# Kernel optimization log

Hardware: AMD Instinct MI355X
Metric: run time of the kernel (lower is better)

The kernel has to match this reference:

```python
import jax, jax.numpy as jnp
import numpy as np

N = 100000   # nodes
E = 3200000  # edges
HIGH, LOW, EMB, HID, OUT = 384, 64, 128, 128, 2

def setup_inputs() -> dict:
    key = jax.random.key(0)
    ks = jax.random.split(key, 12)
    def lin(k, fan_in, fan_out):
        bound = 1.0 / np.sqrt(fan_in)
        kw, kb = jax.random.split(k)
        W = jax.random.uniform(kw, (fan_in, fan_out), jnp.float32, -bound, bound)
        b = jax.random.uniform(kb, (fan_out,), jnp.float32, -bound, bound)
        return W, b
    W_emb, b_emb = lin(ks[0], LOW, EMB)
    W1, b1 = lin(ks[1], HIGH + EMB, HID)
    W2, b2 = lin(ks[2], HID, HID)
    W_lin, b_lin = lin(ks[3], HID, OUT)
    return {
        "high_dim_features": jax.random.normal(ks[4], (N, HIGH), jnp.float32),
        "low_dim_features": jax.random.normal(ks[5], (N, LOW), jnp.float32),
        "edge_index": jax.random.randint(ks[6], (2, E), 0, N, jnp.int32),
        "W_emb": W_emb, "b_emb": b_emb,
        "W1": W1, "b1": b1,
        "W2": W2, "b2": b2,
        "W_lin": W_lin, "b_lin": b_lin,
    }

def _gcn_conv(x, W, b, src, dst, dis):
    # GCNConv: add self-loops, symmetric normalization D^-1/2 (A+I) D^-1/2
    xl = x @ W                                   # [N, out]
    norm = dis[src] * dis[dst]                   # [E]
    agg = jax.ops.segment_sum(xl[src] * norm[:, None], dst, num_segments=N)
    agg = agg + xl * (dis * dis)[:, None]        # self-loop term
    return agg + b

def reference(high_dim_features, low_dim_features, edge_index,
              W_emb, b_emb, W1, b1, W2, b2, W_lin, b_lin):
    src, dst = edge_index[0], edge_index[1]
    # degree with self-loops, computed on destination nodes (PyG default)
    deg = jax.ops.segment_sum(jnp.ones((E,), jnp.float32), dst, num_segments=N) + 1.0
    dis = jax.lax.rsqrt(deg)                     # deg >= 1 always

    low_emb = jax.nn.relu(low_dim_features @ W_emb + b_emb)
    x = jnp.concatenate([high_dim_features, low_emb], axis=1)  # [N, HIGH+EMB]
    x = jax.nn.relu(_gcn_conv(x, W1, b1, src, dst, dis))
    # dropout is identity in eval mode
    x = jax.nn.relu(_gcn_conv(x, W2, b2, src, dst, dis))
    x = x @ W_lin + b_lin
    return jax.nn.log_softmax(x, axis=1)
```

## Files before the change

### kernel.cpp

```cpp
#include <hip/hip_runtime.h>

#define HIGH 384
#define LOWD 64
#define EMB  128
#define HID  128

#define BINSHIFT 8
#define SRCBITS  17
#define SRCMASK  0x1FFFF
#define NBLK     256

typedef unsigned int u32;
typedef unsigned short u16;
typedef unsigned char u8;
typedef __attribute__((ext_vector_type(8))) short bf16x8;
typedef __attribute__((ext_vector_type(4))) float f32x4;
typedef __attribute__((ext_vector_type(2))) float f32x2;

__device__ __forceinline__ u32 pack_bf16(float a, float b) {
    u32 ua = __builtin_bit_cast(u32, a);
    u32 ub = __builtin_bit_cast(u32, b);
    ua += 0x7fffu + ((ua >> 16) & 1u);
    ub += 0x7fffu + ((ub >> 16) & 1u);
    return (ua >> 16) | (ub & 0xffff0000u);
}
__device__ __forceinline__ u16 pack1_bf16(float a) {
    u32 ua = __builtin_bit_cast(u32, a);
    ua += 0x7fffu + ((ua >> 16) & 1u);
    return (u16)(ua >> 16);
}
__device__ __forceinline__ u8 pack1_fp8(float a) {
    int r = __builtin_amdgcn_cvt_pk_fp8_f32(a, a, 0, false);
    return (u8)(r & 0xff);
}


__global__ void k_dis(const int* __restrict__ cnt, float* __restrict__ dis, int N) {
    int i = blockIdx.x * 256 + threadIdx.x;
    if (i < N) dis[i] = rsqrtf((float)cnt[i] + 1.0f);
}

__global__ void k_castw_all(const float* __restrict__ W1, u16* __restrict__ Wt1,
                            const float* __restrict__ W2, u16* __restrict__ Wt2,
                            const float* __restrict__ WE, u16* __restrict__ WtE) {
    int i = blockIdx.x * 256 + threadIdx.x;
    if (i < 65536) {
        int k = i >> 7, c = i & 127;
        Wt1[c * 512 + k] = pack1_bf16(W1[i]);
    } else if (i < 81920) {
        int j = i - 65536;
        int k = j >> 7, c = j & 127;
        Wt2[c * 128 + k] = pack1_bf16(W2[j]);
    } else if (i < 90112) {
        int j = i - 81920;
        int k = j >> 7, c = j & 127;
        WtE[c * 64 + k] = pack1_bf16(WE[j]);
    }
}


__global__ __launch_bounds__(256) void k_binhist(const int* __restrict__ dst, int E,
                                                 int* __restrict__ cnts, int NB) {
    __shared__ int hist[512];
    for (int b = threadIdx.x; b < NB; b += 256) hist[b] = 0;
    __syncthreads();
    int CH = (E + gridDim.x - 1) / gridDim.x;
    int e0 = blockIdx.x * CH;
    int e1 = min(E, e0 + CH);
    for (int e = e0 + threadIdx.x; e < e1; e += 256)
        atomicAdd(&hist[dst[e] >> BINSHIFT], 1);
    __syncthreads();
    for (int b = threadIdx.x; b < NB; b += 256)
        cnts[b * NBLK + blockIdx.x] = hist[b];
}

__global__ __launch_bounds__(256) void k_binscatter(const int* __restrict__ src,
                                                    const int* __restrict__ dst, int E,
                                                    const int* __restrict__ cnts,
                                                    u32* __restrict__ packed, int NB) {
    __shared__ int cur[512];
    for (int b = threadIdx.x; b < NB; b += 256) cur[b] = cnts[b * NBLK + blockIdx.x];
    __syncthreads();
    int CH = (E + gridDim.x - 1) / gridDim.x;
    int e0 = blockIdx.x * CH;
    int e1 = min(E, e0 + CH);
    for (int e = e0 + threadIdx.x; e < e1; e += 256) {
        int d = dst[e];
        int s = src[e];
        int bin = d >> BINSHIFT;
        int pos = atomicAdd(&cur[bin], 1);
        packed[pos] = (u32)s | ((u32)(d & 255) << SRCBITS);
    }
}

__global__ __launch_bounds__(256) void k_hist2(const u32* __restrict__ packed,
                                               const int* __restrict__ cnts, int E,
                                               int* __restrict__ cnt, int NB, int N) {
    __shared__ int hist[256];
    int t = threadIdx.x;
    hist[t] = 0;
    __syncthreads();
    int b = blockIdx.x;
    int begin = cnts[b * NBLK];
    int end = (b + 1 < NB) ? cnts[(b + 1) * NBLK] : E;
    for (int e = begin + t; e < end; e += 256)
        atomicAdd(&hist[packed[e] >> SRCBITS], 1);
    __syncthreads();
    int idx = (b << BINSHIFT) + t;
    if (idx < N) cnt[idx] = hist[t];
}

__global__ __launch_bounds__(256) void k_fill2(const u32* __restrict__ packed,
                                               const int* __restrict__ cnts, int E,
                                               const int* __restrict__ row_start,
                                               int* __restrict__ csr, int NB, int N) {
    __shared__ int cur[256];
    int t = threadIdx.x;
    int b = blockIdx.x;
    int base = b << BINSHIFT;
    cur[t] = row_start[min(base + t, N)];
    __syncthreads();
    int begin = cnts[b * NBLK];
    int end = (b + 1 < NB) ? cnts[(b + 1) * NBLK] : E;
    for (int e = begin + t; e < end; e += 256) {
        u32 p = packed[e];
        int pos = atomicAdd(&cur[p >> SRCBITS], 1);
        csr[pos] = (int)((p & SRCMASK) << 5);
    }
}


__global__ void k_scan1(const int* __restrict__ in, int n, int* __restrict__ bsums) {
    __shared__ int sh[256];
    int t = threadIdx.x;
    int base = blockIdx.x * 1024 + t * 4;
    int s = 0;
#pragma unroll
    for (int j = 0; j < 4; j++) { int idx = base + j; s += (idx < n) ? in[idx] : 0; }
    sh[t] = s; __syncthreads();
    for (int off = 128; off > 0; off >>= 1) {
        if (t < off) sh[t] += sh[t + off];
        __syncthreads();
    }
    if (t == 0) bsums[blockIdx.x] = sh[0];
}

__global__ void k_scan2(int* bsums, int nb) {
    if (threadIdx.x == 0 && blockIdx.x == 0) {
        int run = 0;
        for (int i = 0; i < nb; i++) { int v = bsums[i]; bsums[i] = run; run += v; }
    }
}

__global__ void k_scan3_flat(int* __restrict__ data, int n, const int* __restrict__ bsums) {
    __shared__ int sh[256];
    int t = threadIdx.x;
    int base = blockIdx.x * 1024 + t * 4;
    int v[4]; int s = 0;
#pragma unroll
    for (int j = 0; j < 4; j++) { int idx = base + j; v[j] = (idx < n) ? data[idx] : 0; s += v[j]; }
    sh[t] = s; __syncthreads();
    int x = s;
    for (int off = 1; off < 256; off <<= 1) {
        int y = (t >= off) ? sh[t - off] : 0;
        __syncthreads();
        x += y; sh[t] = x;
        __syncthreads();
    }
    int run = bsums[blockIdx.x] + (x - s);
#pragma unroll
    for (int j = 0; j < 4; j++) {
        int idx = base + j;
        if (idx < n) data[idx] = run;
        run += v[j];
    }
}

__global__ void k_scan3_rows(const int* __restrict__ cnt, int N, const int* __restrict__ bsums,
                             int* __restrict__ row_start, int E) {
    __shared__ int sh[256];
    int t = threadIdx.x;
    int base = blockIdx.x * 1024 + t * 4;
    int v[4]; int s = 0;
#pragma unroll
    for (int j = 0; j < 4; j++) { int idx = base + j; v[j] = (idx < N) ? cnt[idx] : 0; s += v[j]; }
    sh[t] = s; __syncthreads();
    int x = s;
    for (int off = 1; off < 256; off <<= 1) {
        int y = (t >= off) ? sh[t - off] : 0;
        __syncthreads();
        x += y; sh[t] = x;
        __syncthreads();
    }
    int run = bsums[blockIdx.x] + (x - s);
#pragma unroll
    for (int j = 0; j < 4; j++) {
        int idx = base + j;
        if (idx < N) row_start[idx] = run;
        run += v[j];
    }
    if (blockIdx.x == 0 && t == 0) row_start[N] = E;
}


template<bool A1BF, bool BIAS, bool RELU, bool SCALE, int OUT>
__global__ __launch_bounds__(256) void k_mgemm(
    const void* __restrict__ A1v, int K1,
    const u32* __restrict__ A2, int K2,
    const u16* __restrict__ Wt,
    const float* __restrict__ bias,
    const float* __restrict__ dis,
    void* __restrict__ Cv, int M)
{
    __shared__ u32 Als[2][128][16];
    __shared__ u32 Bls[2][128][16];

    const int tid = threadIdx.x;
    const int l = tid & 63;
    const int w = tid >> 6;
    const int g = l >> 4;
    const int lr = l & 15;
    const int blockRow = blockIdx.x * 128;
    const int K = K1 + K2;
    const int T = K >> 5;

    const int sr = tid >> 1;
    const int sh_ = tid & 1;
    int arow = blockRow + sr; if (arow >= M) arow = M - 1;
    const int ssw = (sr >> 1) & 3;
    const int sb0 = (sh_ * 2 + ssw) & 3;
    const int sb1 = (sh_ * 2 + 1 + ssw) & 3;

    const float* a1f = (const float*)A1v + (size_t)arow * K1;
    const u32*   a1b = (const u32*)A1v + (size_t)arow * (K1 >> 1);
    const u32*   a2b = A2 + (size_t)arow * (K2 >> 1);
    const u32*   wtb = (const u32*)Wt + (size_t)sr * (K >> 1);

    f32x4 acc[2][8];
#pragma unroll
    for (int i = 0; i < 2; i++)
#pragma unroll
        for (int j = 0; j < 8; j++) acc[i][j] = (f32x4)0.f;

    u32 pk[8], wk[8];

    auto load_tile = [&](int k0) {
        if (k0 < K1) {
            if (A1BF) {
                const u32* src = a1b + ((k0 + sh_ * 16) >> 1);
                uint4 a = *(const uint4*)src;
                uint4 b = *(const uint4*)(src + 4);
                pk[0] = a.x; pk[1] = a.y; pk[2] = a.z; pk[3] = a.w;
                pk[4] = b.x; pk[5] = b.y; pk[6] = b.z; pk[7] = b.w;
            } else {
                const float* src = a1f + k0 + sh_ * 16;
                float4 f0 = *(const float4*)(src + 0);
                float4 f1 = *(const float4*)(src + 4);
                float4 f2 = *(const float4*)(src + 8);
                float4 f3 = *(const float4*)(src + 12);
                pk[0] = pack_bf16(f0.x, f0.y); pk[1] = pack_bf16(f0.z, f0.w);
                pk[2] = pack_bf16(f1.x, f1.y); pk[3] = pack_bf16(f1.z, f1.w);
                pk[4] = pack_bf16(f2.x, f2.y); pk[5] = pack_bf16(f2.z, f2.w);
                pk[6] = pack_bf16(f3.x, f3.y); pk[7] = pack_bf16(f3.z, f3.w);
            }
        } else {
            const u32* src = a2b + ((k0 - K1 + sh_ * 16) >> 1);
            uint4 a = *(const uint4*)src;
            uint4 b = *(const uint4*)(src + 4);
            pk[0] = a.x; pk[1] = a.y; pk[2] = a.z; pk[3] = a.w;
            pk[4] = b.x; pk[5] = b.y; pk[6] = b.z; pk[7] = b.w;
        }
        const u32* srcw = wtb + ((k0 + sh_ * 16) >> 1);
        uint4 a = *(const uint4*)srcw;
        uint4 b = *(const uint4*)(srcw + 4);
        wk[0] = a.x; wk[1] = a.y; wk[2] = a.z; wk[3] = a.w;
        wk[4] = b.x; wk[5] = b.y; wk[6] = b.z; wk[7] = b.w;
    };
    auto store_tile = [&](int buf) {
        *(uint4*)&Als[buf][sr][sb0 * 4] = make_uint4(pk[0], pk[1], pk[2], pk[3]);
        *(uint4*)&Als[buf][sr][sb1 * 4] = make_uint4(pk[4], pk[5], pk[6], pk[7]);
        *(uint4*)&Bls[buf][sr][sb0 * 4] = make_uint4(wk[0], wk[1], wk[2], wk[3]);
        *(uint4*)&Bls[buf][sr][sb1 * 4] = make_uint4(wk[4], wk[5], wk[6], wk[7]);
    };

    load_tile(0);
    store_tile(0);
    __syncthreads();

    for (int t = 0; t < T; t++) {
        const int cur = t & 1;
        const bool more = (t + 1 < T);
        if (more) load_tile((t + 1) << 5);

        bf16x8 af[2];
#pragma unroll
        for (int rf = 0; rf < 2; rf++) {
            int r = w * 32 + rf * 16 + lr;
            int blk = (g + ((r >> 1) & 3)) & 3;
            af[rf] = *(const bf16x8*)&Als[cur][r][blk * 4];
        }
#pragma unroll
        for (int cb = 0; cb < 8; cb++) {
            int c = cb * 16 + lr;
            int blk = (g + ((c >> 1) & 3)) & 3;
            bf16x8 bf = *(const bf16x8*)&Bls[cur][c][blk * 4];
            acc[0][cb] = __builtin_amdgcn_mfma_f32_16x16x32_bf16(af[0], bf, acc[0][cb], 0, 0, 0);
            acc[1][cb] = __builtin_amdgcn_mfma_f32_16x16x32_bf16(af[1], bf, acc[1][cb], 0, 0, 0);
        }
        if (more) store_tile(cur ^ 1);
        __syncthreads();
    }

    float disv[2][4];
    if (SCALE) {
#pragma unroll
        for (int rf = 0; rf < 2; rf++)
#pragma unroll
            for (int j = 0; j < 4; j++) {
                int row = blockRow + w * 32 + rf * 16 + g * 4 + j;
                disv[rf][j] = (row < M) ? dis[row] : 0.f;
            }
    }
#pragma unroll
    for (int rf = 0; rf < 2; rf++) {
#pragma unroll
        for (int cb = 0; cb < 8; cb++) {
            int col = cb * 16 + lr;
            float bv = BIAS ? bias[col] : 0.f;
#pragma unroll
            for (int j = 0; j < 4; j++) {
                int row = blockRow + w * 32 + rf * 16 + g * 4 + j;
                if (row < M) {
                    float v = acc[rf][cb][j];
                    if (BIAS) v += bv;
                    if (SCALE) v *= disv[rf][j];
                    if (RELU) v = fmaxf(v, 0.f);
                    if (OUT == 0) {
                        ((u16*)Cv)[(size_t)row * 128 + col] = pack1_bf16(v);
                    } else {
                        ((u8*)Cv)[(size_t)row * 128 + col] = pack1_fp8(v);
                    }
                }
            }
        }
    }
}


template<int MODE>
__global__ __launch_bounds__(256) void k_gatherw(
    const u32* __restrict__ xls32, const int* __restrict__ row_start,
    const int* __restrict__ csr, const float* __restrict__ dis,
    const float* __restrict__ bias, const float* __restrict__ Wl,
    const float* __restrict__ bl, void* __restrict__ outv, int N)
{
    int wave = threadIdx.x >> 6;
    int lane = threadIdx.x & 63;
    int half = lane >> 5;
    int w32 = lane & 31;
    int n = blockIdx.x * 4 + wave;
    if (n >= N) return;
    int jb = row_start[n], je = row_start[n + 1];

    float a0 = 0.f, a1 = 0.f, a2 = 0.f, a3 = 0.f;
    {
        u32 v = xls32[(u32)n * 32 + w32];
        if (half == 0) {
            f32x2 lo = __builtin_amdgcn_cvt_pk_f32_fp8((int)v, false);
            f32x2 hi = __builtin_amdgcn_cvt_pk_f32_fp8((int)v, true);
            a0 = lo.x; a1 = lo.y; a2 = hi.x; a3 = hi.y;
        }
    }

    int j = jb;
    for (; j + 7 < je; j += 8) {
        int c0 = csr[j + 4 * half + 0];
        int c1 = csr[j + 4 * half + 1];
        int c2 = csr[j + 4 * half + 2];
        int c3 = csr[j + 4 * half + 3];
        u32 v0 = xls32[(u32)c0 + w32];
        u32 v1 = xls32[(u32)c1 + w32];
        u32 v2 = xls32[(u32)c2 + w32];
        u32 v3 = xls32[(u32)c3 + w32];
        f32x2 l0 = __builtin_amdgcn_cvt_pk_f32_fp8((int)v0, false);
        f32x2 h0 = __builtin_amdgcn_cvt_pk_f32_fp8((int)v0, true);
        f32x2 l1 = __builtin_amdgcn_cvt_pk_f32_fp8((int)v1, false);
        f32x2 h1 = __builtin_amdgcn_cvt_pk_f32_fp8((int)v1, true);
        f32x2 l2 = __builtin_amdgcn_cvt_pk_f32_fp8((int)v2, false);
        f32x2 h2 = __builtin_amdgcn_cvt_pk_f32_fp8((int)v2, true);
        f32x2 l3 = __builtin_amdgcn_cvt_pk_f32_fp8((int)v3, false);
        f32x2 h3 = __builtin_amdgcn_cvt_pk_f32_fp8((int)v3, true);
        a0 += (l0.x + l1.x) + (l2.x + l3.x);
        a1 += (l0.y + l1.y) + (l2.y + l3.y);
        a2 += (h0.x + h1.x) + (h2.x + h3.x);
        a3 += (h0.y + h1.y) + (h2.y + h3.y);
    }
    for (; j + 3 < je; j += 4) {
        int c0 = csr[j + 2 * half];
        int c1 = csr[j + 2 * half + 1];
        u32 v0 = xls32[(u32)c0 + w32];
        u32 v1 = xls32[(u32)c1 + w32];
        f32x2 l0 = __builtin_amdgcn_cvt_pk_f32_fp8((int)v0, false);
        f32x2 h0 = __builtin_amdgcn_cvt_pk_f32_fp8((int)v0, true);
        f32x2 l1 = __builtin_amdgcn_cvt_pk_f32_fp8((int)v1, false);
        f32x2 h1 = __builtin_amdgcn_cvt_pk_f32_fp8((int)v1, true);
        a0 += l0.x + l1.x; a1 += l0.y + l1.y;
        a2 += h0.x + h1.x; a3 += h0.y + h1.y;
    }
    if (j + 1 < je) {
        int c = csr[j + half];
        u32 v = xls32[(u32)c + w32];
        f32x2 lo = __builtin_amdgcn_cvt_pk_f32_fp8((int)v, false);
        f32x2 hi = __builtin_amdgcn_cvt_pk_f32_fp8((int)v, true);
        a0 += lo.x; a1 += lo.y; a2 += hi.x; a3 += hi.y;
        j += 2;
    }
    if (j < je) {
        int c = csr[j];
        u32 v = xls32[(u32)c + w32];
        if (half == 0) {
            f32x2 lo = __builtin_amdgcn_cvt_pk_f32_fp8((int)v, false);
            f32x2 hi = __builtin_amdgcn_cvt_pk_f32_fp8((int)v, true);
            a0 += lo.x; a1 += lo.y; a2 += hi.x; a3 += hi.y;
        }
    }

    a0 += __shfl(a0, w32 + 32);
    a1 += __shfl(a1, w32 + 32);
    a2 += __shfl(a2, w32 + 32);
    a3 += __shfl(a3, w32 + 32);

    float d = dis[n];
    float4 bv = *(const float4*)&bias[w32 * 4];
    float h0v = fmaxf(fmaf(d, a0, bv.x), 0.f);
    float h1v = fmaxf(fmaf(d, a1, bv.y), 0.f);
    float h2v = fmaxf(fmaf(d, a2, bv.z), 0.f);
    float h3v = fmaxf(fmaf(d, a3, bv.w), 0.f);

    if (MODE == 0) {
        if (half == 0) {
            uint2 pw;
            pw.x = pack_bf16(h0v, h1v);
            pw.y = pack_bf16(h2v, h3v);
            *(uint2*)((u32*)outv + (size_t)n * 64 + w32 * 2) = pw;
        }
    } else {
        float4 q0 = *(const float4*)&Wl[w32 * 8];
        float4 q1 = *(const float4*)&Wl[w32 * 8 + 4];
        float p0 = h0v * q0.x + h1v * q0.z + h2v * q1.x + h3v * q1.z;
        float p1 = h0v * q0.y + h1v * q0.w + h2v * q1.y + h3v * q1.w;
#pragma unroll
        for (int off = 16; off > 0; off >>= 1) {
            p0 += __shfl_down(p0, off);
            p1 += __shfl_down(p1, off);
        }
        if (lane == 0) {
            float z0 = p0 + bl[0], z1 = p1 + bl[1];
            float m = fmaxf(z0, z1);
            float ls = m + logf(expf(z0 - m) + expf(z1 - m));
            float* out = (float*)outv;
            out[(size_t)n * 2 + 0] = z0 - ls;
            out[(size_t)n * 2 + 1] = z1 - ls;
        }
    }
}


extern "C" void kernel_launch(void* const* d_in, const int* in_sizes, int n_in,
                              void* d_out, int out_size, void* d_ws, size_t ws_size,
                              hipStream_t stream) {
    const float* high  = (const float*)d_in[0];
    const float* low   = (const float*)d_in[1];
    const int*   ei    = (const int*)d_in[2];
    const float* W_emb = (const float*)d_in[3];
    const float* b_emb = (const float*)d_in[4];
    const float* W1    = (const float*)d_in[5];
    const float* b1    = (const float*)d_in[6];
    const float* W2    = (const float*)d_in[7];
    const float* b2    = (const float*)d_in[8];
    const float* Wl    = (const float*)d_in[9];
    const float* bl    = (const float*)d_in[10];

    int N = in_sizes[0] / HIGH;
    int E = in_sizes[2] / 2;
    const int* srcp = ei;
    const int* dstp = ei + E;
    float* out = (float*)d_out;

    int NB = (N + 255) >> BINSHIFT;
    int NSCAN = NB * NBLK;

    char* ws = (char*)d_ws;
    size_t off = 0;
    auto alloc = [&](size_t b) { size_t o = off; off += (b + 255) & ~(size_t)255; return o; };
    float* dis       = (float*)(ws + alloc((size_t)N * 4));
    int*   cnt       = (int*)  (ws + alloc((size_t)N * 4));
    int*   row_start = (int*)  (ws + alloc((size_t)(N + 1) * 4));
    int*   bsums     = (int*)  (ws + alloc(4096));
    int*   cnts      = (int*)  (ws + alloc((size_t)NSCAN * 4));
    u32*   packed    = (u32*)  (ws + alloc((size_t)E * 4));
    int*   csr       = (int*)  (ws + alloc((size_t)E * 4));
    u16*   Wt1       = (u16*)  (ws + alloc((size_t)512 * 128 * 2));
    u16*   Wt2       = (u16*)  (ws + alloc((size_t)128 * 128 * 2));
    u16*   WtE       = (u16*)  (ws + alloc((size_t)64 * 128 * 2));
    u16*   bufE      = (u16*)  (ws + alloc((size_t)N * 128 * 2));
    u8*    bufX      = (u8*)   (ws + alloc((size_t)N * 128));
    u16*   bufH      = (u16*)  (ws + alloc((size_t)N * 128 * 2));
    (void)ws_size; (void)n_in; (void)out_size;

    int nbS = (NSCAN + 1023) / 1024;
    int nbN = (N + 1023) / 1024;
    int mt  = (N + 127) / 128;

    k_castw_all<<<(90112 + 255) / 256, 256, 0, stream>>>(W1, Wt1, W2, Wt2, W_emb, WtE);

    k_binhist<<<NBLK, 256, 0, stream>>>(dstp, E, cnts, NB);
    k_scan1<<<nbS, 256, 0, stream>>>(cnts, NSCAN, bsums);
    k_scan2<<<1, 64, 0, stream>>>(bsums, nbS);
    k_scan3_flat<<<nbS, 256, 0, stream>>>(cnts, NSCAN, bsums);
    k_binscatter<<<NBLK, 256, 0, stream>>>(srcp, dstp, E, cnts, packed, NB);
    k_hist2<<<NB, 256, 0, stream>>>(packed, cnts, E, cnt, NB, N);
    k_dis<<<(N + 255) / 256, 256, 0, stream>>>(cnt, dis, N);
    k_scan1<<<nbN, 256, 0, stream>>>(cnt, N, bsums);
    k_scan2<<<1, 64, 0, stream>>>(bsums, nbN);
    k_scan3_rows<<<nbN, 256, 0, stream>>>(cnt, N, bsums, row_start, E);
    k_fill2<<<NB, 256, 0, stream>>>(packed, cnts, E, row_start, csr, NB, N);

    k_mgemm<false, true, true, false, 0><<<mt, 256, 0, stream>>>(
        low, LOWD, (const u32*)bufE, 0, WtE, b_emb, nullptr, bufE, N);
    k_mgemm<false, false, false, true, 1><<<mt, 256, 0, stream>>>(
        high, HIGH, (const u32*)bufE, EMB, Wt1, nullptr, dis, bufX, N);
    k_gatherw<0><<<(N + 3) / 4, 256, 0, stream>>>(
        (const u32*)bufX, row_start, csr, dis, b1, nullptr, nullptr, bufH, N);
    k_mgemm<true, false, false, true, 1><<<mt, 256, 0, stream>>>(
        bufH, HID, (const u32*)bufH, 0, Wt2, nullptr, dis, bufX, N);
    k_gatherw<1><<<(N + 3) / 4, 256, 0, stream>>>(
        (const u32*)bufX, row_start, csr, dis, b2, Wl, bl, out, N);
}
```

Baseline: 395.5 us.

## Halve GEMM row tile to 64 rows for more blocks and occupancy

The fused MFMA GEMM kernel now computes a 64-row tile per block instead of 128. Each wave handles one 16-row fragment instead of two, and the A-tile load mapping is reworked to four threads per row. Launch bounds request six blocks per CU. The intent is to launch more blocks and raise occupancy and latency hiding on the many-CU GPU. The cost is that each block reuses the loaded weight tile over fewer rows, so weight traffic to LDS doubles and there are fewer MFMAs per sync.

```diff
diff --git a/kernel.cpp b/kernel.cpp
--- a/kernel.cpp
+++ b/kernel.cpp
@@ -204,7 +204,7 @@
 
 
 template<bool A1BF, bool BIAS, bool RELU, bool SCALE, int OUT>
-__global__ __launch_bounds__(256) void k_mgemm(
+__global__ __launch_bounds__(256, 6) void k_mgemm(
     const void* __restrict__ A1v, int K1,
     const u32* __restrict__ A2, int K2,
     const u16* __restrict__ Wt,
@@ -212,7 +212,7 @@
     const float* __restrict__ dis,
     void* __restrict__ Cv, int M)
 {
-    __shared__ u32 Als[2][128][16];
+    __shared__ u32 Als[2][64][16];
     __shared__ u32 Bls[2][128][16];
 
     const int tid = threadIdx.x;
@@ -220,67 +220,58 @@
     const int w = tid >> 6;
     const int g = l >> 4;
     const int lr = l & 15;
-    const int blockRow = blockIdx.x * 128;
+    const int blockRow = blockIdx.x * 64;
     const int K = K1 + K2;
     const int T = K >> 5;
 
-    const int sr = tid >> 1;
-    const int sh_ = tid & 1;
-    int arow = blockRow + sr; if (arow >= M) arow = M - 1;
-    const int ssw = (sr >> 1) & 3;
-    const int sb0 = (sh_ * 2 + ssw) & 3;
-    const int sb1 = (sh_ * 2 + 1 + ssw) & 3;
+    const int ar = tid >> 2;
+    const int ak = tid & 3;
+    int arow = blockRow + ar; if (arow >= M) arow = M - 1;
+    const int awb = (ak + ((ar >> 1) & 3)) & 3;
+
+    const int wc = tid >> 1;
+    const int wh = tid & 1;
+    const int wsw = (wc >> 1) & 3;
+    const int wb0 = (wh * 2 + wsw) & 3;
+    const int wb1 = (wh * 2 + 1 + wsw) & 3;
 
     const float* a1f = (const float*)A1v + (size_t)arow * K1;
     const u32*   a1b = (const u32*)A1v + (size_t)arow * (K1 >> 1);
     const u32*   a2b = A2 + (size_t)arow * (K2 >> 1);
-    const u32*   wtb = (const u32*)Wt + (size_t)sr * (K >> 1);
-
-    f32x4 acc[2][8];
-#pragma unroll
-    for (int i = 0; i < 2; i++)
-#pragma unroll
-        for (int j = 0; j < 8; j++) acc[i][j] = (f32x4)0.f;
-
-    u32 pk[8], wk[8];
+    const u32*   wtb = (const u32*)Wt + (size_t)wc * (K >> 1);
+
+    f32x4 acc[8];
+#pragma unroll
+    for (int j = 0; j < 8; j++) acc[j] = (f32x4)0.f;
+
+    u32 pa[4], wk[8];
 
     auto load_tile = [&](int k0) {
         if (k0 < K1) {
             if (A1BF) {
-                const u32* src = a1b + ((k0 + sh_ * 16) >> 1);
-                uint4 a = *(const uint4*)src;
-                uint4 b = *(const uint4*)(src + 4);
-                pk[0] = a.x; pk[1] = a.y; pk[2] = a.z; pk[3] = a.w;
-                pk[4] = b.x; pk[5] = b.y; pk[6] = b.z; pk[7] = b.w;
+                uint4 a = *(const uint4*)(a1b + (k0 >> 1) + ak * 4);
+                pa[0] = a.x; pa[1] = a.y; pa[2] = a.z; pa[3] = a.w;
             } else {
-                const float* src = a1f + k0 + sh_ * 16;
+                const float* src = a1f + k0 + ak * 8;
                 float4 f0 = *(const float4*)(src + 0);
                 float4 f1 = *(const float4*)(src + 4);
-                float4 f2 = *(const float4*)(src + 8);
-                float4 f3 = *(const float4*)(src + 12);
-                pk[0] = pack_bf16(f0.x, f0.y); pk[1] = pack_bf16(f0.z, f0.w);
-                pk[2] = pack_bf16(f1.x, f1.y); pk[3] = pack_bf16(f1.z, f1.w);
-                pk[4] = pack_bf16(f2.x, f2.y); pk[5] = pack_bf16(f2.z, f2.w);
-                pk[6] = pack_bf16(f3.x, f3.y); pk[7] = pack_bf16(f3.z, f3.w);
+                pa[0] = pack_bf16(f0.x, f0.y); pa[1] = pack_bf16(f0.z, f0.w);
+                pa[2] = pack_bf16(f1.x, f1.y); pa[3] = pack_bf16(f1.z, f1.w);
             }
         } else {
-            const u32* src = a2b + ((k0 - K1 + sh_ * 16) >> 1);
-            uint4 a = *(const uint4*)src;
-            uint4 b = *(const uint4*)(src + 4);
-            pk[0] = a.x; pk[1] = a.y; pk[2] = a.z; pk[3] = a.w;
-            pk[4] = b.x; pk[5] = b.y; pk[6] = b.z; pk[7] = b.w;
-        }
-        const u32* srcw = wtb + ((k0 + sh_ * 16) >> 1);
+            uint4 a = *(const uint4*)(a2b + ((k0 - K1) >> 1) + ak * 4);
+            pa[0] = a.x; pa[1] = a.y; pa[2] = a.z; pa[3] = a.w;
+        }
+        const u32* srcw = wtb + ((k0 + wh * 16) >> 1);
         uint4 a = *(const uint4*)srcw;
         uint4 b = *(const uint4*)(srcw + 4);
         wk[0] = a.x; wk[1] = a.y; wk[2] = a.z; wk[3] = a.w;
         wk[4] = b.x; wk[5] = b.y; wk[6] = b.z; wk[7] = b.w;
     };
     auto store_tile = [&](int buf) {
-        *(uint4*)&Als[buf][sr][sb0 * 4] = make_uint4(pk[0], pk[1], pk[2], pk[3]);
-        *(uint4*)&Als[buf][sr][sb1 * 4] = make_uint4(pk[4], pk[5], pk[6], pk[7]);
-        *(uint4*)&Bls[buf][sr][sb0 * 4] = make_uint4(wk[0], wk[1], wk[2], wk[3]);
-        *(uint4*)&Bls[buf][sr][sb1 * 4] = make_uint4(wk[4], wk[5], wk[6], wk[7]);
+        *(uint4*)&Als[buf][ar][awb * 4] = make_uint4(pa[0], pa[1], pa[2], pa[3]);
+        *(uint4*)&Bls[buf][wc][wb0 * 4] = make_uint4(wk[0], wk[1], wk[2], wk[3]);
+        *(uint4*)&Bls[buf][wc][wb1 * 4] = make_uint4(wk[4], wk[5], wk[6], wk[7]);
     };
 
     load_tile(0);
@@ -292,54 +283,47 @@
         const bool more = (t + 1 < T);
         if (more) load_tile((t + 1) << 5);
 
-        bf16x8 af[2];
-#pragma unroll
-        for (int rf = 0; rf < 2; rf++) {
-            int r = w * 32 + rf * 16 + lr;
+        bf16x8 af;
+        {
+            int r = w * 16 + lr;
             int blk = (g + ((r >> 1) & 3)) & 3;
-            af[rf] = *(const bf16x8*)&Als[cur][r][blk * 4];
+            af = *(const bf16x8*)&Als[cur][r][blk * 4];
         }
 #pragma unroll
         for (int cb = 0; cb < 8; cb++) {
             int c = cb * 16 + lr;
             int blk = (g + ((c >> 1) & 3)) & 3;
             bf16x8 bf = *(const bf16x8*)&Bls[cur][c][blk * 4];
-            acc[0][cb] = __builtin_amdgcn_mfma_f32_16x16x32_bf16(af[0], bf, acc[0][cb], 0, 0, 0);
-            acc[1][cb] = __builtin_amdgcn_mfma_f32_16x16x32_bf16(af[1], bf, acc[1][cb], 0, 0, 0);
+            acc[cb] = __builtin_amdgcn_mfma_f32_16x16x32_bf16(af, bf, acc[cb], 0, 0, 0);
         }
         if (more) store_tile(cur ^ 1);
         __syncthreads();
     }
 
-    float disv[2][4];
+    float disv[4];
     if (SCALE) {
 #pragma unroll
-        for (int rf = 0; rf < 2; rf++)
-#pragma unroll
-            for (int j = 0; j < 4; j++) {
-                int row = blockRow + w * 32 + rf * 16 + g * 4 + j;
-                disv[rf][j] = (row < M) ? dis[row] : 0.f;
-            }
-    }
-#pragma unroll
-    for (int rf = 0; rf < 2; rf++) {
-#pragma unroll
-        for (int cb = 0; cb < 8; cb++) {
-            int col = cb * 16 + lr;
-            float bv = BIAS ? bias[col] : 0.f;
-#pragma unroll
-            for (int j = 0; j < 4; j++) {
-                int row = blockRow + w * 32 + rf * 16 + g * 4 + j;
-                if (row < M) {
-                    float v = acc[rf][cb][j];
-                    if (BIAS) v += bv;
-                    if (SCALE) v *= disv[rf][j];
-                    if (RELU) v = fmaxf(v, 0.f);
-                    if (OUT == 0) {
-                        ((u16*)Cv)[(size_t)row * 128 + col] = pack1_bf16(v);
-                    } else {
-                        ((u8*)Cv)[(size_t)row * 128 + col] = pack1_fp8(v);
-                    }
+        for (int j = 0; j < 4; j++) {
+            int row = blockRow + w * 16 + g * 4 + j;
+            disv[j] = (row < M) ? dis[row] : 0.f;
+        }
+    }
+#pragma unroll
+    for (int cb = 0; cb < 8; cb++) {
+        int col = cb * 16 + lr;
+        float bv = BIAS ? bias[col] : 0.f;
+#pragma unroll
+        for (int j = 0; j < 4; j++) {
+            int row = blockRow + w * 16 + g * 4 + j;
+            if (row < M) {
+                float v = acc[cb][j];
+                if (BIAS) v += bv;
+                if (SCALE) v *= disv[j];
+                if (RELU) v = fmaxf(v, 0.f);
+                if (OUT == 0) {
+                    ((u16*)Cv)[(size_t)row * 128 + col] = pack1_bf16(v);
+                } else {
+                    ((u8*)Cv)[(size_t)row * 128 + col] = pack1_fp8(v);
                 }
             }
         }
@@ -510,7 +494,7 @@
 
     int nbS = (NSCAN + 1023) / 1024;
     int nbN = (N + 1023) / 1024;
-    int mt  = (N + 127) / 128;
+    int mt  = (N + 63) / 64;
 
     k_castw_all<<<(90112 + 255) / 256, 256, 0, stream>>>(W1, Wt1, W2, Wt2, W_emb, WtE);
 
```

Measured after the change: 371.8 us. -6.0%, faster.
